# Performance work log

Measured on AMD Instinct MI355X. Metric: run time of the kernel, lower is better.

The kernel has to match this reference:

```python
import jax, jax.numpy as jnp
import numpy as np

N = 32768       # batch of states
DQ = 8          # q_ndim (dof_ndim)
A = 4           # action_dim
H = 1024        # hidden_size


def setup_inputs() -> dict:
    key = jax.random.key(0)
    ks = jax.random.split(key, 16)

    def lin(kw, kb, fan_out, fan_in, zero_bias=False):
        s = 1.0 / np.sqrt(fan_in)
        W = jax.random.normal(kw, (fan_out, fan_in), dtype=jnp.float32) * s
        b = jnp.zeros((fan_out,), jnp.float32) if zero_bias else \
            jax.random.normal(kb, (fan_out,), dtype=jnp.float32) * s
        return W, b

    W1, b1 = lin(ks[0], ks[1], H, 2 * DQ)            # h_net layer 1
    W2, b2 = lin(ks[2], ks[3], H, H)                 # h_net layer 2
    Wh, bh = lin(ks[4], ks[5], 1, H)                 # h_net head -> scalar H(z)
    Wf1, bf1 = lin(ks[6], ks[7], H, 2 * DQ + A)      # flex_net layer 1
    Wf2, bf2 = lin(ks[8], ks[9], H, H)               # flex_net layer 2
    Wff, bff = lin(ks[10], ks[11], 2 * DQ, H)        # flex_net head -> 2*q_ndim
    Wp, bp = lin(ks[12], ks[13], A, 2 * DQ)          # control policy (detached)

    return {
        "t": jnp.zeros((), jnp.float32),
        "z": jax.random.normal(ks[14], (N, 2 * DQ), dtype=jnp.float32),
        "W1": W1, "b1": b1, "W2": W2, "b2": b2, "Wh": Wh, "bh": bh,
        "Wf1": Wf1, "bf1": bf1, "Wf2": Wf2, "bf2": bf2, "Wff": Wff, "bff": bff,
        "Wp": Wp, "bp": bp,
    }


def reference(t, z, W1, b1, W2, b2, Wh, bh,
              Wf1, bf1, Wf2, bf2, Wff, bff, Wp, bp):
    # control input, detached as in the torch forward (u = policy(t, z).detach())
    u = jax.lax.stop_gradient(jnp.tanh(z @ Wp.T + bp))  # [N, A]

    # ---- H-net forward, saving tanh' at each activation (the `sps` list) ----
    # angular_dims=() -> CosSin is the identity, so h_net[0](z) = z.
    a1 = z @ W1.T + b1          # [N, H]
    h1 = jnp.tanh(a1)
    s0 = 1.0 - h1 * h1          # d tanh / d a1   (sps[0])
    a2 = h1 @ W2.T + b2         # [N, H]
    h2 = jnp.tanh(a2)
    s1 = 1.0 - h2 * h2          # d tanh / d a2   (sps[1])

    # dH = grad_z sum(h_net(z)), with gradients flowing (create_graph=True)
    def H_sum(zz):
        hh = jnp.tanh(zz @ W1.T + b1)
        hh = jnp.tanh(hh @ W2.T + b2)
        return jnp.sum(hh @ Wh.T + bh)

    dH = jax.grad(H_sum)(z)     # [N, 2*DQ]

    # ---- flex-net with skip term modulated by reversed tanh' maps ----
    zu = jnp.concatenate([z, u], axis=-1)       # [N, 2*DQ + A]
    f1 = zu @ Wf1.T + bf1
    g1 = jnp.tanh(f1) + f1 * s1                 # idx = 1 -> sps[1]
    f2 = g1 @ Wf2.T + bf2
    g2 = jnp.tanh(f2) + f2 * s0                 # idx = 0 -> sps[0]
    out = g2 @ Wff.T + bff                      # [N, 2*DQ]

    # D = jacobian of CosSin = identity per batch row (angular_dims=()), so
    # bmm(out[:,None,:], D).squeeze(1) == out.

    # dz_dt = J @ (out + dH):  J([top; bot]) = [bot; -top]
    s = out + dH
    return jnp.concatenate([s[:, DQ:], -s[:, :DQ]], axis=-1)  # [N, 2*DQ]
```

## Files before the change

### kernel.cpp

```cpp
#include <hip/hip_runtime.h>
#include <hip/hip_bf16.h>

typedef __hip_bfloat16 bf16;
typedef __attribute__((ext_vector_type(8))) short short8;
typedef __attribute__((ext_vector_type(4))) short s16x4;
typedef __attribute__((ext_vector_type(4))) float f32x4;

__device__ __forceinline__ bf16 f2b(float f) { return __float2bfloat16(f); }
__device__ __forceinline__ short bfbits(float f) {
  union { float f; unsigned u; } x; x.f = f;
  unsigned r = x.u + 0x7fff + ((x.u >> 16) & 1);
  return (short)(r >> 16);
}
__device__ __forceinline__ float tanh_fast(float x) {
  float t = __expf(-2.f * fabsf(x));
  float r = (1.f - t) * __builtin_amdgcn_rcpf(1.f + t);
  return copysignf(r, x);
}

#define BM 128
#define BN 128
#define BK 32

#define GLOAD_LDS16(gp, lp) __builtin_amdgcn_global_load_lds( \
    (const __attribute__((address_space(1))) void*)(gp), \
    (__attribute__((address_space(3))) void*)(lp), 16, 0, 0)

__global__ __launch_bounds__(256) void prep(
    const float* __restrict__ W2, const float* __restrict__ Wf2,
    const float* __restrict__ W1, const float* __restrict__ Wff,
    bf16* __restrict__ W2bf, bf16* __restrict__ W2Tbf,
    bf16* __restrict__ Wf2bf, bf16* __restrict__ W1n,
    bf16* __restrict__ Wffn)
{
  __shared__ float T[32][33];
  const int tid = threadIdx.x, bx = blockIdx.x;
  const int tx = bx & 31, ty = bx >> 5;
  const int r = tid >> 3, c4 = (tid & 7) * 4;
  const long ibase = (long)(ty * 32 + r) * 1024 + tx * 32 + c4;

  f32x4 v = *(const f32x4*)(W2 + ibase);
  f32x4 vf = *(const f32x4*)(Wf2 + ibase);
  s16x4 sv, sf;
  #pragma unroll
  for (int j = 0; j < 4; ++j) {
    sv[j] = bfbits(v[j]); sf[j] = bfbits(vf[j]);
    T[r][c4 + j] = v[j];
  }
  *(s16x4*)(W2bf + ibase) = sv;
  *(s16x4*)(Wf2bf + ibase) = sf;
  __syncthreads();
  const int oc = tid >> 3, or4 = (tid & 7) * 4;
  s16x4 st;
  #pragma unroll
  for (int j = 0; j < 4; ++j) st[j] = bfbits(T[or4 + j][oc]);
  *(s16x4*)(W2Tbf + (long)(tx * 32 + oc) * 1024 + ty * 32 + or4) = st;

  if (bx < 32) {
    #pragma unroll
    for (int rep = 0; rep < 2; ++rep) {
      int i = bx * 512 + rep * 256 + tid;
      int rr = i >> 10, cc = i & 1023;
      W1n[i] = f2b(W1[cc * 16 + rr]);
      Wffn[i] = f2b(Wff[i]);
    }
  }
}

__global__ __launch_bounds__(256) void k1(
    const float* __restrict__ z, const float* __restrict__ W1,
    const float* __restrict__ b1, const float* __restrict__ Wp,
    const float* __restrict__ bp, const float* __restrict__ Wf1,
    const float* __restrict__ bf1v,
    bf16* __restrict__ h1, bf16* __restrict__ f1out, long grow0)
{
  __shared__ float zs[32][16];
  __shared__ float us[32][4];
  const int tid = threadIdx.x;
  const long r0 = (long)blockIdx.x * 32;
  for (int i = tid; i < 512; i += 256) {
    int r = i >> 4, c = i & 15;
    zs[r][c] = z[(grow0 + r0 + r) * 16 + c];
  }
  __syncthreads();
  if (tid < 128) {
    int r = tid >> 2, a = tid & 3;
    float acc = bp[a];
    #pragma unroll
    for (int k = 0; k < 16; ++k) acc = fmaf(zs[r][k], Wp[a * 16 + k], acc);
    us[r][a] = tanh_fast(acc);
  }
  __syncthreads();
  #pragma unroll
  for (int jj = 0; jj < 4; ++jj) {
    const int c = tid + jj * 256;
    {
      float w[16];
      #pragma unroll
      for (int k = 0; k < 16; ++k) w[k] = W1[c * 16 + k];
      const float bc = b1[c];
      for (int r = 0; r < 32; ++r) {
        float a = bc;
        #pragma unroll
        for (int k = 0; k < 16; ++k) a = fmaf(zs[r][k], w[k], a);
        h1[(r0 + r) * 1024 + c] = f2b(tanh_fast(a));
      }
    }
    {
      float wf[20];
      #pragma unroll
      for (int k = 0; k < 20; ++k) wf[k] = Wf1[c * 20 + k];
      const float bfc = bf1v[c];
      for (int r = 0; r < 32; ++r) {
        float f = bfc;
        #pragma unroll
        for (int k = 0; k < 16; ++k) f = fmaf(zs[r][k], wf[k], f);
        #pragma unroll
        for (int a = 0; a < 4; ++a) f = fmaf(us[r][a], wf[16 + a], f);
        f1out[(r0 + r) * 1024 + c] = f2b(f);
      }
    }
  }
}

template<int EPI>
__global__ __launch_bounds__(256) void gemm_k(
    const bf16* __restrict__ A, const bf16* __restrict__ Bp,
    const float* __restrict__ bias, const float* __restrict__ Whv,
    const bf16* __restrict__ h1, const bf16* __restrict__ f1g,
    bf16* __restrict__ O1, bf16* __restrict__ O2,
    const bf16* __restrict__ Wn, float* __restrict__ Pp, int ckRows)
{
  constexpr int SMEM = (EPI == 0) ? 16384 : 34816;
  __shared__ __align__(16) char smem[SMEM];
  bf16* As = (bf16*)smem;
  bf16* Bs = (bf16*)(smem + 8192);
  const int tid = threadIdx.x;
  const int lane = tid & 63, wid = tid >> 6;
  const int wr = wid >> 1, wc = wid & 1;
  const int fr = lane & 15, kg = lane >> 4;
  const long row0 = (long)blockIdx.x * BM;
  const int col0 = blockIdx.y * BN;

  const int sr0 = tid >> 2;
  const int sk0 = ((tid & 3) ^ ((tid >> 3) & 3)) * 8;
  const int swr = (fr >> 1) & 3;

  f32x4 acc[4][4];
  #pragma unroll
  for (int m = 0; m < 4; ++m)
    #pragma unroll
    for (int n = 0; n < 4; ++n) acc[m][n] = (f32x4){0.f, 0.f, 0.f, 0.f};

  for (int kt = 0; kt < 1024 / BK; ++kt) {
    const int k0 = kt * BK;
    #pragma unroll
    for (int it = 0; it < 2; ++it) {
      const bf16* ga = A + (row0 + sr0 + it * 64) * 1024 + (k0 + sk0);
      GLOAD_LDS16(ga, As + it * 2048 + tid * 8);
      const bf16* gbp = Bp + (long)(col0 + sr0 + it * 64) * 1024 + (k0 + sk0);
      GLOAD_LDS16(gbp, Bs + it * 2048 + tid * 8);
    }
    __syncthreads();
    short8 af[4], bfr[4];
    #pragma unroll
    for (int m = 0; m < 4; ++m)
      af[m] = *(const short8*)(As + (wr * 64 + m * 16 + fr) * 32 + (kg ^ swr) * 8);
    #pragma unroll
    for (int n = 0; n < 4; ++n)
      bfr[n] = *(const short8*)(Bs + (wc * 64 + n * 16 + fr) * 32 + (kg ^ swr) * 8);
    #pragma unroll
    for (int m = 0; m < 4; ++m)
      #pragma unroll
      for (int n = 0; n < 4; ++n)
        acc[m][n] = __builtin_amdgcn_mfma_f32_16x16x32_bf16(af[m], bfr[n], acc[m][n], 0, 0, 0);
    __syncthreads();
  }

  if (EPI == 0) {
    #pragma unroll
    for (int m = 0; m < 4; ++m) {
      const long gr0 = row0 + wr * 64 + m * 16 + kg * 4;
      #pragma unroll
      for (int n = 0; n < 4; ++n) {
        const int gc = col0 + wc * 64 + n * 16 + fr;
        const float b2c = bias[gc], whc = Whv[gc];
        f32x4 v = acc[m][n];
        #pragma unroll
        for (int j = 0; j < 4; ++j) {
          const long idx = (gr0 + j) * 1024 + gc;
          float h = tanh_fast(v[j] + b2c);
          float s1v = 1.f - h * h;
          float f = __bfloat162float(f1g[idx]);
          O2[idx] = f2b(s1v * whc);
          O1[idx] = f2b(tanh_fast(f) + f * s1v);
        }
      }
    }
  } else {
    bf16* Ot = (bf16*)smem;
    #pragma unroll
    for (int m = 0; m < 4; ++m) {
      const int rl0 = wr * 64 + m * 16 + kg * 4;
      const long gr0 = row0 + rl0;
      #pragma unroll
      for (int n = 0; n < 4; ++n) {
        const int cl = wc * 64 + n * 16 + fr;
        const int gc = col0 + cl;
        f32x4 v = acc[m][n];
        #pragma unroll
        for (int j = 0; j < 4; ++j) {
          const long idx = (gr0 + j) * 1024 + gc;
          float x = v[j];
          if (EPI == 1) {
            float hh = __bfloat162float(h1[idx]);
            Ot[(rl0 + j) * 136 + cl] = f2b(x * (1.f - hh * hh));
          } else {
            float f = x + bias[gc];
            float hh = __bfloat162float(h1[idx]);
            Ot[(rl0 + j) * 136 + cl] = f2b(tanh_fast(f) + f * (1.f - hh * hh));
          }
        }
      }
    }
    __syncthreads();
    #pragma unroll
    for (int sub = 0; sub < 2; ++sub) {
      const int rl0 = wid * 32 + sub * 16;
      f32x4 pacc = (f32x4){0.f, 0.f, 0.f, 0.f};
      #pragma unroll
      for (int ks = 0; ks < 4; ++ks) {
        short8 afrag = *(const short8*)(Ot + (rl0 + fr) * 136 + ks * 32 + kg * 8);
        short8 bfrag = *(const short8*)(Wn + fr * 1024 + col0 + ks * 32 + kg * 8);
        pacc = __builtin_amdgcn_mfma_f32_16x16x32_bf16(afrag, bfrag, pacc, 0, 0, 0);
      }
      #pragma unroll
      for (int j = 0; j < 4; ++j)
        Pp[((long)blockIdx.y * ckRows + row0 + rl0 + kg * 4 + j) * 16 + fr] = pacc[j];
    }
  }
}

__global__ __launch_bounds__(256) void k7(
    const float* __restrict__ Pp0, const float* __restrict__ Pp1,
    const float* __restrict__ bff, float* __restrict__ out,
    long grow0, int ckRows)
{
  int i = blockIdx.x * 256 + threadIdx.x;
  int r = i >> 4, j = i & 15, jp = (j + 8) & 15;
  float s = bff[jp];
  #pragma unroll
  for (int cb = 0; cb < 8; ++cb) {
    long o = ((long)cb * ckRows + r) * 16 + jp;
    s += Pp0[o] + Pp1[o];
  }
  out[(grow0 + r) * 16 + j] = (j < 8) ? s : -s;
}

extern "C" void kernel_launch(void* const* d_in, const int* in_sizes, int n_in,
                              void* d_out, int out_size, void* d_ws, size_t ws_size,
                              hipStream_t stream) {
  const float* z   = (const float*)d_in[1];
  const float* W1  = (const float*)d_in[2];
  const float* b1  = (const float*)d_in[3];
  const float* W2  = (const float*)d_in[4];
  const float* b2  = (const float*)d_in[5];
  const float* Wh  = (const float*)d_in[6];
  const float* Wf1 = (const float*)d_in[8];
  const float* bf1 = (const float*)d_in[9];
  const float* Wf2 = (const float*)d_in[10];
  const float* bf2 = (const float*)d_in[11];
  const float* Wff = (const float*)d_in[12];
  const float* bff = (const float*)d_in[13];
  const float* Wp  = (const float*)d_in[14];
  const float* bp  = (const float*)d_in[15];
  float* out = (float*)d_out;
  const int N = in_sizes[1] / 16;

  char* p = (char*)d_ws;
  auto alloc = [&](size_t bytes) {
    char* q = p; p += (bytes + 255) & ~(size_t)255; return q;
  };
  bf16* W2bf  = (bf16*)alloc(1024 * 1024 * 2);
  bf16* W2Tbf = (bf16*)alloc(1024 * 1024 * 2);
  bf16* Wf2bf = (bf16*)alloc(1024 * 1024 * 2);
  bf16* W1n   = (bf16*)alloc(16 * 1024 * 2);
  bf16* Wffn  = (bf16*)alloc(16 * 1024 * 2);
  size_t wbytes = (size_t)(p - (char*)d_ws);

  int CK = N;
  while (CK > 128 && wbytes + (size_t)CK * 9216 > ws_size) CK >>= 1;
  bf16* actA = (bf16*)alloc((size_t)CK * 2048);
  bf16* actB = (bf16*)alloc((size_t)CK * 2048);
  bf16* actD = (bf16*)alloc((size_t)CK * 2048);
  bf16* actE = (bf16*)alloc((size_t)CK * 2048);
  float* Pp0 = (float*)alloc((size_t)CK * 8 * 16 * 4);
  float* Pp1 = (float*)alloc((size_t)CK * 8 * 16 * 4);

  prep<<<1024, 256, 0, stream>>>(W2, Wf2, W1, Wff, W2bf, W2Tbf, Wf2bf, W1n, Wffn);

  for (long r0 = 0; r0 < N; r0 += CK) {
    k1<<<CK / 32, 256, 0, stream>>>(z, W1, b1, Wp, bp, Wf1, bf1, actA, actE, r0);
    gemm_k<0><<<dim3(CK / 128, 8), 256, 0, stream>>>(
        actA, W2bf, b2, Wh, nullptr, actE, actD, actB, nullptr, nullptr, CK);
    gemm_k<1><<<dim3(CK / 128, 8), 256, 0, stream>>>(
        actB, W2Tbf, nullptr, nullptr, actA, nullptr, nullptr, nullptr,
        W1n, Pp0, CK);
    gemm_k<2><<<dim3(CK / 128, 8), 256, 0, stream>>>(
        actD, Wf2bf, bf2, nullptr, actA, nullptr, nullptr, nullptr,
        Wffn, Pp1, CK);
    k7<<<CK / 16, 256, 0, stream>>>(Pp0, Pp1, bff, out, r0, CK);
  }
}
```

Before: 406.5 us.

## Double-buffer LDS tiles in GEMM mainloop and reuse f1 buffer in place

The GEMM main loop now ping-pongs between two LDS stages. It issues the global-to-LDS loads for tile k+1 before the MFMAs on tile k, so memory latency can overlap with compute. This doubles the LDS footprint of the EPI 0 variant, which may reduce occupancy. Separately, the first epilogue now reads f1 from the same buffer it overwrites with g1, and the actE workspace buffer is dropped. That shrinks per-row workspace so larger chunks may fit.

```diff
diff --git a/kernel.cpp b/kernel.cpp
--- a/kernel.cpp
+++ b/kernel.cpp
@@ -127,14 +127,12 @@
 __global__ __launch_bounds__(256) void gemm_k(
     const bf16* __restrict__ A, const bf16* __restrict__ Bp,
     const float* __restrict__ bias, const float* __restrict__ Whv,
-    const bf16* __restrict__ h1, const bf16* __restrict__ f1g,
-    bf16* __restrict__ O1, bf16* __restrict__ O2,
+    const bf16* __restrict__ h1,
+    bf16* O1, bf16* __restrict__ O2,
     const bf16* __restrict__ Wn, float* __restrict__ Pp, int ckRows)
 {
-  constexpr int SMEM = (EPI == 0) ? 16384 : 34816;
+  constexpr int SMEM = (EPI == 0) ? 32768 : 34816;
   __shared__ __align__(16) char smem[SMEM];
-  bf16* As = (bf16*)smem;
-  bf16* Bs = (bf16*)(smem + 8192);
   const int tid = threadIdx.x;
   const int lane = tid & 63, wid = tid >> 6;
   const int wr = wid >> 1, wc = wid & 1;
@@ -146,29 +144,36 @@
   const int sk0 = ((tid & 3) ^ ((tid >> 3) & 3)) * 8;
   const int swr = (fr >> 1) & 3;
 
-  f32x4 acc[4][4];
-  #pragma unroll
-  for (int m = 0; m < 4; ++m)
-    #pragma unroll
-    for (int n = 0; n < 4; ++n) acc[m][n] = (f32x4){0.f, 0.f, 0.f, 0.f};
-
-  for (int kt = 0; kt < 1024 / BK; ++kt) {
-    const int k0 = kt * BK;
+  const bf16* gA = A + (row0 + sr0) * 1024 + sk0;
+  const bf16* gB = Bp + ((long)col0 + sr0) * 1024 + sk0;
+
+  auto STAGE = [&](int buf, int k0) {
+    bf16* as = (bf16*)smem + buf * 4096;
+    bf16* bs = (bf16*)smem + 8192 + buf * 4096;
     #pragma unroll
     for (int it = 0; it < 2; ++it) {
-      const bf16* ga = A + (row0 + sr0 + it * 64) * 1024 + (k0 + sk0);
-      GLOAD_LDS16(ga, As + it * 2048 + tid * 8);
-      const bf16* gbp = Bp + (long)(col0 + sr0 + it * 64) * 1024 + (k0 + sk0);
-      GLOAD_LDS16(gbp, Bs + it * 2048 + tid * 8);
-    }
-    __syncthreads();
+      GLOAD_LDS16(gA + (long)it * 64 * 1024 + k0, as + it * 2048 + tid * 8);
+      GLOAD_LDS16(gB + (long)it * 64 * 1024 + k0, bs + it * 2048 + tid * 8);
+    }
+  };
+
+  f32x4 acc[4][4] = {};
+
+  STAGE(0, 0);
+  __syncthreads();
+
+  for (int kt = 0; kt < 32; ++kt) {
+    const int cur = kt & 1;
+    if (kt < 31) STAGE(cur ^ 1, (kt + 1) * 32);
+    const bf16* as = (const bf16*)smem + cur * 4096;
+    const bf16* bs = (const bf16*)smem + 8192 + cur * 4096;
     short8 af[4], bfr[4];
     #pragma unroll
     for (int m = 0; m < 4; ++m)
-      af[m] = *(const short8*)(As + (wr * 64 + m * 16 + fr) * 32 + (kg ^ swr) * 8);
+      af[m] = *(const short8*)(as + (wr * 64 + m * 16 + fr) * 32 + (kg ^ swr) * 8);
     #pragma unroll
     for (int n = 0; n < 4; ++n)
-      bfr[n] = *(const short8*)(Bs + (wc * 64 + n * 16 + fr) * 32 + (kg ^ swr) * 8);
+      bfr[n] = *(const short8*)(bs + (wc * 64 + n * 16 + fr) * 32 + (kg ^ swr) * 8);
     #pragma unroll
     for (int m = 0; m < 4; ++m)
       #pragma unroll
@@ -191,7 +196,7 @@
           const long idx = (gr0 + j) * 1024 + gc;
           float h = tanh_fast(v[j] + b2c);
           float s1v = 1.f - h * h;
-          float f = __bfloat162float(f1g[idx]);
+          float f = __bfloat162float(((const bf16*)O1)[idx]);
           O2[idx] = f2b(s1v * whc);
           O1[idx] = f2b(tanh_fast(f) + f * s1v);
         }
@@ -289,26 +294,23 @@
   size_t wbytes = (size_t)(p - (char*)d_ws);
 
   int CK = N;
-  while (CK > 128 && wbytes + (size_t)CK * 9216 > ws_size) CK >>= 1;
+  while (CK > 128 && wbytes + (size_t)CK * 7168 > ws_size) CK >>= 1;
   bf16* actA = (bf16*)alloc((size_t)CK * 2048);
   bf16* actB = (bf16*)alloc((size_t)CK * 2048);
   bf16* actD = (bf16*)alloc((size_t)CK * 2048);
-  bf16* actE = (bf16*)alloc((size_t)CK * 2048);
   float* Pp0 = (float*)alloc((size_t)CK * 8 * 16 * 4);
   float* Pp1 = (float*)alloc((size_t)CK * 8 * 16 * 4);
 
   prep<<<1024, 256, 0, stream>>>(W2, Wf2, W1, Wff, W2bf, W2Tbf, Wf2bf, W1n, Wffn);
 
   for (long r0 = 0; r0 < N; r0 += CK) {
-    k1<<<CK / 32, 256, 0, stream>>>(z, W1, b1, Wp, bp, Wf1, bf1, actA, actE, r0);
+    k1<<<CK / 32, 256, 0, stream>>>(z, W1, b1, Wp, bp, Wf1, bf1, actA, actD, r0);
     gemm_k<0><<<dim3(CK / 128, 8), 256, 0, stream>>>(
-        actA, W2bf, b2, Wh, nullptr, actE, actD, actB, nullptr, nullptr, CK);
+        actA, W2bf, b2, Wh, nullptr, actD, actB, nullptr, nullptr, CK);
     gemm_k<1><<<dim3(CK / 128, 8), 256, 0, stream>>>(
-        actB, W2Tbf, nullptr, nullptr, actA, nullptr, nullptr, nullptr,
-        W1n, Pp0, CK);
+        actB, W2Tbf, nullptr, nullptr, actA, nullptr, nullptr, W1n, Pp0, CK);
     gemm_k<2><<<dim3(CK / 128, 8), 256, 0, stream>>>(
-        actD, Wf2bf, bf2, nullptr, actA, nullptr, nullptr, nullptr,
-        Wffn, Pp1, CK);
+        actD, Wf2bf, bf2, nullptr, actA, nullptr, nullptr, Wffn, Pp1, CK);
     k7<<<CK / 16, 256, 0, stream>>>(Pp0, Pp1, bff, out, r0, CK);
   }
 }
```

New measurement: 414.7 us. 1.02x slower.
